# Kernel optimization log

Measured on AMD Instinct MI355X. Metric: run time of the kernel, lower is better.

## Reference

```python
import jax, jax.numpy as jnp
import numpy as np

RF = 13          # receptive field with defaults
N_LAYERS = 8     # blocks(4) * layers(2)
DIMS = 32
RC = 16          # residual/dilation channels
SC = 8           # skip channels
BN_EPS = 1e-5


def conv1x1(x, W, b=None):
    # x: (B,Cin,N,T), W: (Cout,Cin)
    y = jnp.einsum('oc,bcnt->bont', W, x)
    if b is not None:
        y = y + b[None, :, None, None]
    return y


def bn_eval(x, g, b):
    # eval-mode BatchNorm2d with running_mean=0, running_var=1
    return x * (g / jnp.sqrt(1.0 + BN_EPS))[None, :, None, None] + b[None, :, None, None]


def setup_inputs() -> dict:
    key = jax.random.key(0)
    ks = jax.random.split(key, 24)
    B, N, T, days = 16, 1024, 12, 288
    inp = {}
    inp['inputs'] = jax.random.normal(ks[0], (B, 2, N, T), dtype=jnp.float32)
    inp['ind'] = jax.random.randint(ks[1], (B,), 0, days)
    # start convs (1 -> RC)
    inp['start_w'] = jax.random.normal(ks[2], (RC, 1)) * 0.05
    inp['start_b'] = jax.random.normal(ks[3], (RC,)) * 0.05
    inp['starta_w'] = jax.random.normal(ks[4], (RC, 1)) * 0.05
    inp['starta_b'] = jax.random.normal(ks[5], (RC,)) * 0.05
    # dynamic-graph node embeddings (torch.randn init)
    inp['p1'] = jax.random.normal(ks[6], (days, DIMS))
    inp['p2'] = jax.random.normal(ks[7], (N, DIMS))
    inp['p3'] = jax.random.normal(ks[8], (N, DIMS))
    inp['pk'] = jax.random.normal(ks[9], (DIMS, DIMS, DIMS))
    # shared channel-attention fcs (bias=False)
    inp['fc1_w'] = jax.random.normal(ks[10], (RC, RC)) * 0.05
    inp['fc2_w'] = jax.random.normal(ks[11], (RC, RC)) * 0.05
    # per-layer skip convs (RC -> SC)
    inp['skip_w'] = jax.random.normal(ks[12], (N_LAYERS, SC, RC)) * 0.05
    inp['skip_b'] = jax.random.normal(ks[13], (N_LAYERS, SC)) * 0.05
    # per-layer gcn mlp ((order*support_len+1)*RC = 48 -> RC)
    inp['gconv_w'] = jax.random.normal(ks[14], (N_LAYERS, RC, 3 * RC)) * 0.05
    inp['gconv_b'] = jax.random.normal(ks[15], (N_LAYERS, RC)) * 0.05
    # batchnorm affine params
    inp['bn_g'] = jnp.ones((N_LAYERS, RC)) + jax.random.normal(ks[16], (N_LAYERS, RC)) * 0.01
    inp['bn_b'] = jax.random.normal(ks[17], (N_LAYERS, RC)) * 0.01
    inp['bna_g'] = jnp.ones((N_LAYERS, RC)) + jax.random.normal(ks[18], (N_LAYERS, RC)) * 0.01
    inp['bna_b'] = jax.random.normal(ks[19], (N_LAYERS, RC)) * 0.01
    # end convs: 832 -> 64 -> 12
    inp['end1_w'] = jax.random.normal(ks[20], (64, SC * RF * N_LAYERS)) * 0.02
    inp['end1_b'] = jax.random.normal(ks[21], (64,)) * 0.02
    inp['end2_w'] = jax.random.normal(ks[22], (12, 64)) * 0.02
    inp['end2_b'] = jax.random.normal(ks[23], (12,)) * 0.02
    return inp


def reference(inputs, ind, start_w, start_b, starta_w, starta_b, p1, p2, p3, pk,
              fc1_w, fc2_w, skip_w, skip_b, gconv_w, gconv_b,
              bn_g, bn_b, bna_g, bna_b, end1_w, end1_b, end2_w, end2_b):
    B, _, N, T = inputs.shape
    if T < RF:  # static python condition
        xo = jnp.pad(inputs, ((0, 0), (0, 0), (0, 0), (RF - T, 0)))
    else:
        xo = inputs
    x = conv1x1(xo[:, 0:1], start_w, start_b)      # (B,RC,N,RF)
    x_a = conv1x1(xo[:, 1:2], starta_w, starta_b)  # (B,RC,N,RF)

    # dgconstruct: dynamic adjacency (identical for every layer -> compute once)
    te = p1[ind]                                   # (B,DIMS)
    adp = jnp.einsum('ai,ijk->ajk', te, pk)        # (B,DIMS,DIMS)
    src = jnp.einsum('bj,ajk->abk', p2, adp)       # (B,N,DIMS)
    full = jnp.einsum('ck,abk->abc', p3, src)      # (B,N,N)
    temp = full[:, :, :DIMS]                       # (B,N,DIMS)
    x1 = jnp.einsum('bnd,bmd->bnm', src, temp)     # (B,N,N)
    A = jax.nn.relu(jnp.tanh(x1 - jnp.swapaxes(x1, 1, 2)))  # x2 = x1^T

    skips = []
    for i in range(N_LAYERS):
        residual = x
        # avg-pool / max-pool to same size are identity -> avg_out == max_out
        a_out = conv1x1(jax.nn.relu(conv1x1(residual, fc1_w)), fc2_w)
        x = jax.nn.sigmoid(a_out + a_out + x)
        residual_a = x_a
        s = conv1x1(x, skip_w[i], skip_b[i])        # (B,SC,N,RF)
        skips.append(jnp.transpose(s, (0, 1, 3, 2)).reshape(B, SC * RF, N, 1))
        # gcn with support_len=1, order=2 (dropout off in eval)
        h1 = jnp.einsum('bcvl,bwv->bcwl', x, A)
        h2 = jnp.einsum('bcvl,bwv->bcwl', h1, A)
        h = jnp.concatenate([x, h1, h2], axis=1)    # (B,3*RC,N,RF)
        x = conv1x1(h, gconv_w[i], gconv_b[i])
        x = x_a + x
        x_a = x_a + residual_a
        x = x + residual
        x = bn_eval(x, bn_g[i], bn_b[i])
        x_a = bn_eval(x_a, bna_g[i], bna_b[i])

    # torch prepends each new skip: last layer's skip goes first
    skip = jnp.concatenate(skips[::-1], axis=1)     # (B,832,N,1)
    out = jax.nn.relu(skip)
    out = jax.nn.relu(conv1x1(out, end1_w, end1_b))
    out = conv1x1(out, end2_w, end2_b)              # (B,12,N,1)
    return out
```

## Files before the change

### kernel.cpp

```cpp
#include <hip/hip_runtime.h>
#include <math.h>

#define NB 16
#define NCH 16
#define NL 13
#define NN 1024
#define NT 12
#define NLAY 8
#define MROWS 208
#define MPAD 256

typedef _Float16 f16;
typedef __attribute__((ext_vector_type(8))) _Float16 f16x8;
typedef __attribute__((ext_vector_type(16))) float f32x16;

#define OFF_TAB   0
#define OFF_ADP   1024
#define OFF_M     (OFF_ADP  + (size_t)NB*1024)
#define OFF_SRC   (OFF_M    + (size_t)NB*1024)
#define OFF_TEMP  (OFF_SRC  + (size_t)NB*NN*32)
#define OFF_AH    (OFF_TEMP + (size_t)NB*NN*32)
#define OFF_XH    (OFF_AH   + (size_t)NB*NN*NN/2)
#define OFF_XL    (OFF_XH   + (size_t)NB*MPAD*NN/2)
#define OFF_H1H   (OFF_XL   + (size_t)NB*MPAD*NN/2)
#define OFF_H1L   (OFF_H1H  + (size_t)NB*MPAD*NN/2)
#define OFF_H2    (OFF_H1L  + (size_t)NB*MPAD*NN/2)
#define OFF_X     (OFF_H2   + (size_t)NB*MPAD*NN)
#define OFF_SKIP  (OFF_X    + (size_t)NB*MROWS*NN)
#define WS_FLOATS (OFF_SKIP + (size_t)NB*832*NN)

__device__ __forceinline__ void gload16(const void* g, void* l) {
    __builtin_amdgcn_global_load_lds(
        (const __attribute__((address_space(1))) unsigned int*)g,
        (__attribute__((address_space(3))) unsigned int*)l,
        16, 0, 0);
}

__device__ __forceinline__ float fast_tanh(float x) {
    float e = __expf(2.0f * x);
    return 1.0f - 2.0f / (e + 1.0f);
}

__global__ void k_tables(const float* __restrict__ bn_g,
                         const float* __restrict__ bna_g, const float* __restrict__ bna_b,
                         const float* __restrict__ sa_w, const float* __restrict__ sa_b,
                         float* __restrict__ tab) {
    int c = threadIdx.x;
    if (c >= 16) return;
    float inv = 1.0f / sqrtf(1.0f + 1e-5f);
    float A = sa_w[c], Bc = sa_b[c];
    for (int i = 0; i < NLAY; i++) {
        tab[i*16 + c]       = bn_g[i*16 + c] * inv;
        tab[128 + i*16 + c] = A;
        tab[256 + i*16 + c] = Bc;
        float ga = bna_g[i*16 + c] * inv;
        A  = 2.0f * ga * A;
        Bc = 2.0f * ga * Bc + bna_b[i*16 + c];
    }
}

__global__ __launch_bounds__(256) void k_startfc(const float* __restrict__ inp,
                        const float* __restrict__ sw, const float* __restrict__ sb,
                        const float* __restrict__ fc1, const float* __restrict__ fc2,
                        const float* __restrict__ skw, const float* __restrict__ skb,
                        float* __restrict__ x, f16* __restrict__ xh, f16* __restrict__ xl,
                        float* __restrict__ skip) {
    int t = threadIdx.x;
    int idx = blockIdx.x*256 + t;
    int n = idx & 1023;
    int q = idx >> 10;
    int l = q % 13, b = q / 13;
    float u = (l == 0) ? 0.f : inp[((size_t)(b*2 + 0)*NN + n)*NT + (l - 1)];
    float v[16], t1[16], v2[16];
    #pragma unroll
    for (int c = 0; c < 16; c++) {
        v[c] = sw[c]*u + sb[c];
        x[((size_t)b*MROWS + c*13 + l)*NN + n] = v[c];
    }
    #pragma unroll
    for (int c = 0; c < 16; c++) {
        float s = 0.f;
        #pragma unroll
        for (int j = 0; j < 16; j++) s += fc1[c*16 + j] * v[j];
        t1[c] = fmaxf(s, 0.f);
    }
    #pragma unroll
    for (int c = 0; c < 16; c++) {
        float s = 0.f;
        #pragma unroll
        for (int j = 0; j < 16; j++) s += fc2[c*16 + j] * t1[j];
        float z = 2.f*s + v[c];
        v2[c] = 1.f / (1.f + __expf(-z));
        size_t o = ((size_t)b*MPAD + c*13 + l)*NN + n;
        f16 hi = (f16)v2[c];
        xh[o] = hi;
        xl[o] = (f16)(v2[c] - (float)hi);
    }
    #pragma unroll
    for (int sc = 0; sc < 8; sc++) {
        float s = skb[sc];
        #pragma unroll
        for (int c = 0; c < 16; c++) s += skw[sc*16 + c] * v2[c];
        skip[((size_t)b*832 + 7*104 + sc*13 + l)*NN + n] = s;
    }
}

__global__ __launch_bounds__(256) void k_adp(const float* __restrict__ p1, const int* __restrict__ ind,
                      const float* __restrict__ pk, const float* __restrict__ p3,
                      float* __restrict__ adpg, float* __restrict__ Mg) {
    __shared__ float te[32];
    __shared__ float adp[32][32];
    __shared__ float p3s[32][32];
    int b = blockIdx.x, t = threadIdx.x;
    if (t < 32) te[t] = p1[(size_t)ind[b]*32 + t];
    for (int i = t; i < 1024; i += 256) p3s[i >> 5][i & 31] = p3[i];
    __syncthreads();
    for (int i = t; i < 1024; i += 256) {
        float s = 0.f;
        for (int q = 0; q < 32; q++) s += te[q] * pk[q*1024 + i];
        adp[i >> 5][i & 31] = s;
        adpg[(size_t)b*1024 + i] = s;
    }
    __syncthreads();
    for (int i = t; i < 1024; i += 256) {
        int j = i >> 5, c = i & 31;
        float s = 0.f;
        for (int k = 0; k < 32; k++) s += adp[j][k] * p3s[c][k];
        Mg[(size_t)b*1024 + i] = s;
    }
}

__global__ __launch_bounds__(256) void k_st(const float* __restrict__ p2, const float* __restrict__ adpg,
                     const float* __restrict__ Mg,
                     float* __restrict__ src, float* __restrict__ temp) {
    __shared__ float adpS[32][32], MS[32][32], p2S[128][32];
    int b = blockIdx.y, n0 = blockIdx.x * 128, t = threadIdx.x;
    for (int i = t; i < 1024; i += 256) {
        adpS[i >> 5][i & 31] = adpg[(size_t)b*1024 + i];
        MS[i >> 5][i & 31]   = Mg[(size_t)b*1024 + i];
    }
    for (int i = t; i < 128*32; i += 256) p2S[i >> 5][i & 31] = p2[(size_t)(n0 + (i >> 5))*32 + (i & 31)];
    __syncthreads();
    int k = t & 31, g = t >> 5;
    for (int nn = g; nn < 128; nn += 8) {
        float rs = 0.f, rt = 0.f;
        #pragma unroll 8
        for (int j = 0; j < 32; j++) {
            float pv = p2S[nn][j];
            rs += pv * adpS[j][k];
            rt += pv * MS[j][k];
        }
        src [((size_t)b*NN + n0 + nn)*32 + k] = rs;
        temp[((size_t)b*NN + n0 + nn)*32 + k] = rt;
    }
}

__global__ __launch_bounds__(256) void k_A(const float* __restrict__ src, const float* __restrict__ temp,
                    f16* __restrict__ Amat) {
    int b = blockIdx.z;
    int r = blockIdx.x, ti = 0;
    while (r >= 16 - ti) { r -= 16 - ti; ti++; }
    int tj = ti + r;
    int n0 = ti*64, m0 = tj*64;
    __shared__ float snT[32][68], tmT[32][68], smT[32][68], tnT[32][68];
    __shared__ f16 At[64][72];
    int t = threadIdx.x;
    const float* sb_ = src  + (size_t)b*NN*32;
    const float* tb_ = temp + (size_t)b*NN*32;
    for (int i = t; i < 64*32; i += 256) {
        int rr = i >> 5, k = i & 31;
        snT[k][rr] = sb_[(n0 + rr)*32 + k];
        tmT[k][rr] = tb_[(m0 + rr)*32 + k];
        smT[k][rr] = sb_[(m0 + rr)*32 + k];
        tnT[k][rr] = tb_[(n0 + rr)*32 + k];
    }
    __syncthreads();
    int tr = (t >> 4) * 4, tc = (t & 15) * 4;
    float acc1[4][4] = {}, acc2[4][4] = {};
    #pragma unroll 4
    for (int k = 0; k < 32; k++) {
        float4 a  = *(const float4*)&snT[k][tr];
        float4 bb = *(const float4*)&tmT[k][tc];
        float4 c2 = *(const float4*)&smT[k][tc];
        float4 d2 = *(const float4*)&tnT[k][tr];
        float av[4] = {a.x, a.y, a.z, a.w};
        float bv[4] = {bb.x, bb.y, bb.z, bb.w};
        float cv[4] = {c2.x, c2.y, c2.z, c2.w};
        float dv[4] = {d2.x, d2.y, d2.z, d2.w};
        #pragma unroll
        for (int i = 0; i < 4; i++)
            #pragma unroll
            for (int jj = 0; jj < 4; jj++) { acc1[i][jj] += av[i]*bv[jj]; acc2[i][jj] += cv[jj]*dv[i]; }
    }
    #pragma unroll
    for (int i = 0; i < 4; i++)
        #pragma unroll
        for (int jj = 0; jj < 4; jj++) {
            float v = fast_tanh(acc1[i][jj] - acc2[i][jj]);
            Amat[((size_t)b*NN + n0 + tr + i)*NN + m0 + tc + jj] = (f16)(v > 0.f ? v : 0.f);
            At[tc + jj][tr + i] = (f16)(-v > 0.f ? -v : 0.f);
        }
    __syncthreads();
    for (int i = t; i < 512; i += 256) {
        int rr = i >> 3, c8 = (i & 7) * 8;
        f16* dst = &Amat[((size_t)b*NN + m0 + rr)*NN + n0 + c8];
        #pragma unroll
        for (int k = 0; k < 8; k++) dst[k] = At[rr][c8 + k];
    }
}

template<bool HOP1>
__global__ __launch_bounds__(256) void k_gmm(const f16* __restrict__ Xh, const f16* __restrict__ Xl,
                     const f16* __restrict__ Ag, float* __restrict__ Cf,
                     f16* __restrict__ Ch, f16* __restrict__ Cl) {
    __shared__ alignas(16) f16 As[2][128*64];
    __shared__ alignas(16) f16 Xs[2][2*64*64];
    const int bid = blockIdx.x;
    const int xcd = bid & 7;
    const int j   = bid >> 3;
    const int b   = xcd + ((j >> 5) << 3);
    const int tile = j & 31;
    const int my  = tile >> 3;
    const int n0  = (tile & 7) * 128;
    const int t = threadIdx.x;
    const int w = t >> 6, lane = t & 63;
    const char* Ab  = (const char*)(Ag + (size_t)b*NN*NN);
    const char* Xhb = (const char*)(Xh + (size_t)b*MPAD*NN);
    const char* Xlb = (const char*)(Xl + (size_t)b*MPAD*NN);

    const char* asrc[4];
    int adst[4];
    const char* xsrc[4];
    int xdst[4];
    {
        const char* Abase = Ab + (size_t)n0*2048;
        const char* Xb0 = Xhb + (size_t)(my*64)*2048;
        const char* Xb1 = Xlb + (size_t)(my*64)*2048;
        #pragma unroll
        for (int rr = 0; rr < 4; ++rr) {
            int q = rr*4 + w;
            int slot = q*64 + lane;
            int row = slot >> 3, ch = slot & 7;
            asrc[rr] = Abase + (size_t)row*2048 + ((ch ^ (row & 7)) << 4);
            adst[rr] = q*1024;
            int xrow = row & 63;
            xsrc[rr] = ((q >> 3) ? Xb1 : Xb0) + (size_t)xrow*2048 + ((ch ^ (xrow & 7)) << 4);
            xdst[rr] = q*1024;
        }
    }

    const int wm = (w >> 1) * 32, wn = (w & 1) * 64;
    const int kh = lane >> 5;
    const int arow = wm + (lane & 31);
    const int brow0 = wn + (lane & 31);
    const int brow1 = brow0 + 32;
    const int swa = arow & 7, swb0 = brow0 & 7, swb1 = brow1 & 7;

    f32x16 acc0 = {}, acc1 = {};

    auto stage = [&](int buf, int it) {
        size_t koff = (size_t)it * 128;
        #pragma unroll
        for (int rr = 0; rr < 4; ++rr)
            gload16(asrc[rr] + koff, (char*)As[buf] + adst[rr]);
        #pragma unroll
        for (int rr = 0; rr < 4; ++rr)
            gload16(xsrc[rr] + koff, (char*)Xs[buf] + xdst[rr]);
    };
    auto compute = [&](int buf) {
        const char* aP0 = (const char*)Xs[buf] + (size_t)arow*128;
        const char* aP1 = aP0 + 8192;
        const char* bP0 = (const char*)As[buf] + (size_t)brow0*128;
        const char* bP1 = (const char*)As[buf] + (size_t)brow1*128;
        #pragma unroll
        for (int s = 0; s < 4; ++s) {
            int cn = s*2 + kh;
            f16x8 ah = *(const f16x8*)(aP0 + ((cn ^ swa) << 4));
            f16x8 al = *(const f16x8*)(aP1 + ((cn ^ swa) << 4));
            f16x8 b0 = *(const f16x8*)(bP0 + ((cn ^ swb0) << 4));
            f16x8 b1 = *(const f16x8*)(bP1 + ((cn ^ swb1) << 4));
            acc0 = __builtin_amdgcn_mfma_f32_32x32x16_f16(ah, b0, acc0, 0, 0, 0);
            acc1 = __builtin_amdgcn_mfma_f32_32x32x16_f16(ah, b1, acc1, 0, 0, 0);
            acc0 = __builtin_amdgcn_mfma_f32_32x32x16_f16(al, b0, acc0, 0, 0, 0);
            acc1 = __builtin_amdgcn_mfma_f32_32x32x16_f16(al, b1, acc1, 0, 0, 0);
        }
    };

    stage(0, 0);
    int cur = 0;
    for (int it = 0; it < 15; ++it) {
        stage(cur ^ 1, it + 1);
        asm volatile("s_waitcnt vmcnt(8)" ::: "memory");
        __builtin_amdgcn_s_barrier();
        compute(cur);
        __builtin_amdgcn_s_barrier();
        cur ^= 1;
    }
    asm volatile("s_waitcnt vmcnt(0)" ::: "memory");
    __builtin_amdgcn_s_barrier();
    compute(cur);

    const int coll = lane & 31;
    #pragma unroll
    for (int reg = 0; reg < 16; ++reg) {
        int m = my*64 + wm + (reg & 3) + 8*(reg >> 2) + 4*kh;
        if (m < MROWS) {
            size_t o0 = ((size_t)b*MPAD + m)*NN + n0 + wn + coll;
            float v0 = acc0[reg], v1 = acc1[reg];
            if (HOP1) {
                f16 h0 = (f16)v0; Ch[o0]      = h0; Cl[o0]      = (f16)(v0 - (float)h0);
                f16 h1 = (f16)v1; Ch[o0 + 32] = h1; Cl[o0 + 32] = (f16)(v1 - (float)h1);
            } else {
                Cf[o0] = v0; Cf[o0 + 32] = v1;
            }
        }
    }
}

__global__ __launch_bounds__(256) void k_epifc(float* __restrict__ x,
                      f16* __restrict__ xh, f16* __restrict__ xl,
                      const f16* __restrict__ h1h, const f16* __restrict__ h1l,
                      const float* __restrict__ h2,
                      const float* __restrict__ inp, const float* __restrict__ gw,
                      const float* __restrict__ gb, const float* __restrict__ bnb,
                      const float* __restrict__ tab,
                      const float* __restrict__ fc1, const float* __restrict__ fc2,
                      const float* __restrict__ skw, const float* __restrict__ skb,
                      float* __restrict__ skip, int layer) {
    int t = threadIdx.x;
    const int nl = layer + 1;
    const float* Wg  = gw  + layer*768;
    const float* GB  = gb  + layer*16;
    const float* BNB = bnb + layer*16;
    const float* BNS = tab + layer*16;
    const float* AC  = tab + 128 + layer*16;
    const float* BC  = tab + 256 + layer*16;
    const float* W3  = skw + nl*128;
    const float* B3  = skb + nl*8;

    int idx = blockIdx.x*256 + t;
    int n = idx & 1023;
    int q = idx >> 10;
    int l = q % 13, b = q / 13;
    float u1 = (l == 0) ? 0.f : inp[((size_t)(b*2 + 1)*NN + n)*NT + (l - 1)];
    float vx[16], v1[16], v2[16], xnew[16];
    #pragma unroll
    for (int c = 0; c < 16; c++) {
        size_t op = ((size_t)b*MPAD + c*13 + l)*NN + n;
        vx[c] = (float)xh[op] + (float)xl[op];
        v1[c] = (float)h1h[op] + (float)h1l[op];
        v2[c] = h2[op];
    }
    #pragma unroll
    for (int o = 0; o < 16; o++) {
        float s = GB[o];
        #pragma unroll
        for (int c = 0; c < 16; c++) s += Wg[o*48 + c]      * vx[c];
        #pragma unroll
        for (int c = 0; c < 16; c++) s += Wg[o*48 + 16 + c] * v1[c];
        #pragma unroll
        for (int c = 0; c < 16; c++) s += Wg[o*48 + 32 + c] * v2[c];
        float xa = AC[o]*u1 + BC[o];
        float vo = x[((size_t)b*MROWS + o*13 + l)*NN + n];
        xnew[o] = BNS[o]*(s + xa + vo) + BNB[o];
    }
    if (layer < 6) {
        #pragma unroll
        for (int o = 0; o < 16; o++)
            x[((size_t)b*MROWS + o*13 + l)*NN + n] = xnew[o];
    }
    float t1[16], vs[16];
    #pragma unroll
    for (int c = 0; c < 16; c++) {
        float s = 0.f;
        #pragma unroll
        for (int j = 0; j < 16; j++) s += fc1[c*16 + j] * xnew[j];
        t1[c] = fmaxf(s, 0.f);
    }
    #pragma unroll
    for (int c = 0; c < 16; c++) {
        float s = 0.f;
        #pragma unroll
        for (int j = 0; j < 16; j++) s += fc2[c*16 + j] * t1[j];
        float z = 2.f*s + xnew[c];
        vs[c] = 1.f / (1.f + __expf(-z));
        if (layer < 6) {
            size_t o = ((size_t)b*MPAD + c*13 + l)*NN + n;
            f16 hi = (f16)vs[c];
            xh[o] = hi;
            xl[o] = (f16)(vs[c] - (float)hi);
        }
    }
    #pragma unroll
    for (int sc = 0; sc < 8; sc++) {
        float s = B3[sc];
        #pragma unroll
        for (int c = 0; c < 16; c++) s += W3[sc*16 + c] * vs[c];
        skip[((size_t)b*832 + (7 - nl)*104 + sc*13 + l)*NN + n] = s;
    }
}

__global__ __launch_bounds__(256) void k_end1(const float* __restrict__ skip, const float* __restrict__ w1,
                       float* __restrict__ out1) {
    __shared__ alignas(16) float Ws[52][68];
    __shared__ alignas(16) float Ss[52][68];
    int n0 = blockIdx.x * 64, ks = blockIdx.y, b = blockIdx.z;
    int t = threadIdx.x, ty = t >> 4, tx = t & 15;
    float acc[4][4] = {};
    int kbase = ks * 208;
    for (int kk = 0; kk < 4; kk++) {
        int k0 = kbase + kk*52;
        for (int i = t; i < 52*64; i += 256) {
            int r = i >> 6, c = i & 63;
            float sv = skip[((size_t)b*832 + k0 + r)*NN + n0 + c];
            Ss[r][c] = sv > 0.f ? sv : 0.f;
            Ws[r][c] = w1[(size_t)c*832 + k0 + r];
        }
        __syncthreads();
        #pragma unroll 4
        for (int k = 0; k < 52; k++) {
            float4 av = *(const float4*)&Ws[k][ty*4];
            float4 bv = *(const float4*)&Ss[k][tx*4];
            float a[4] = {av.x, av.y, av.z, av.w};
            float bb[4] = {bv.x, bv.y, bv.z, bv.w};
            #pragma unroll
            for (int i = 0; i < 4; i++)
                #pragma unroll
                for (int jj = 0; jj < 4; jj++) acc[i][jj] += a[i]*bb[jj];
        }
        __syncthreads();
    }
    #pragma unroll
    for (int i = 0; i < 4; i++)
        #pragma unroll
        for (int jj = 0; jj < 4; jj++)
            out1[(((size_t)ks*NB + b)*64 + ty*4 + i)*NN + n0 + tx*4 + jj] = acc[i][jj];
}

__global__ __launch_bounds__(256) void k_end2(const float* __restrict__ out1, const float* __restrict__ b1,
                       const float* __restrict__ w2, const float* __restrict__ b2,
                       float* __restrict__ outp) {
    __shared__ float S[64][68];
    int n0 = blockIdx.x * 64, b = blockIdx.y;
    int t = threadIdx.x;
    for (int i = t; i < 4096; i += 256) {
        int o = i >> 6, n = i & 63;
        float s = b1[o];
        #pragma unroll
        for (int ks = 0; ks < 4; ks++)
            s += out1[(((size_t)ks*NB + b)*64 + o)*NN + n0 + n];
        S[o][n] = s > 0.f ? s : 0.f;
    }
    __syncthreads();
    for (int idx = t; idx < 12*64; idx += 256) {
        int jr = idx >> 6, n = idx & 63;
        float s = b2[jr];
        for (int o = 0; o < 64; o++) s += w2[jr*64 + o] * S[o][n];
        outp[((size_t)b*12 + jr)*NN + n0 + n] = s;
    }
}

extern "C" void kernel_launch(void* const* d_in, const int* in_sizes, int n_in,
                              void* d_out, int out_size, void* d_ws, size_t ws_size,
                              hipStream_t stream) {
    (void)in_sizes; (void)n_in; (void)out_size;
    if (ws_size < WS_FLOATS * sizeof(float)) return;

    const float* inputs  = (const float*)d_in[0];
    const int*   ind     = (const int*)  d_in[1];
    const float* start_w = (const float*)d_in[2];
    const float* start_b = (const float*)d_in[3];
    const float* starta_w= (const float*)d_in[4];
    const float* starta_b= (const float*)d_in[5];
    const float* p1      = (const float*)d_in[6];
    const float* p2      = (const float*)d_in[7];
    const float* p3      = (const float*)d_in[8];
    const float* pk      = (const float*)d_in[9];
    const float* fc1_w   = (const float*)d_in[10];
    const float* fc2_w   = (const float*)d_in[11];
    const float* skip_w  = (const float*)d_in[12];
    const float* skip_b  = (const float*)d_in[13];
    const float* gconv_w = (const float*)d_in[14];
    const float* gconv_b = (const float*)d_in[15];
    const float* bn_g    = (const float*)d_in[16];
    const float* bn_b    = (const float*)d_in[17];
    const float* bna_g   = (const float*)d_in[18];
    const float* bna_b   = (const float*)d_in[19];
    const float* end1_w  = (const float*)d_in[20];
    const float* end1_b  = (const float*)d_in[21];
    const float* end2_w  = (const float*)d_in[22];
    const float* end2_b  = (const float*)d_in[23];

    float* ws   = (float*)d_ws;
    float* tab  = ws + OFF_TAB;
    float* adpg = ws + OFF_ADP;
    float* Mg   = ws + OFF_M;
    float* src  = ws + OFF_SRC;
    float* temp = ws + OFF_TEMP;
    f16*   Ah   = (f16*)(ws + OFF_AH);
    f16*   xh   = (f16*)(ws + OFF_XH);
    f16*   xl   = (f16*)(ws + OFF_XL);
    f16*   h1h  = (f16*)(ws + OFF_H1H);
    f16*   h1l  = (f16*)(ws + OFF_H1L);
    float* h2   = ws + OFF_H2;
    float* x    = ws + OFF_X;
    float* skip = ws + OFF_SKIP;

    k_tables<<<1, 64, 0, stream>>>(bn_g, bna_g, bna_b, starta_w, starta_b, tab);
    k_startfc<<<(NB*NL*NN)/256, 256, 0, stream>>>(inputs, start_w, start_b, fc1_w, fc2_w,
                                                  skip_w, skip_b, x, xh, xl, skip);
    k_adp<<<NB, 256, 0, stream>>>(p1, ind, pk, p3, adpg, Mg);
    k_st<<<dim3(8, NB), 256, 0, stream>>>(p2, adpg, Mg, src, temp);
    k_A<<<dim3(136, 1, NB), 256, 0, stream>>>(src, temp, Ah);

    for (int i = 0; i < 7; i++) {
        k_gmm<true ><<<512, 256, 0, stream>>>(xh,  xl,  Ah, nullptr, h1h, h1l);
        k_gmm<false><<<512, 256, 0, stream>>>(h1h, h1l, Ah, h2, nullptr, nullptr);
        k_epifc<<<(NB*NL*NN)/256, 256, 0, stream>>>(x, xh, xl, h1h, h1l, h2, inputs,
                                                    gconv_w, gconv_b, bn_b, tab,
                                                    fc1_w, fc2_w, skip_w, skip_b, skip, i);
    }
    k_end1<<<dim3(16, 4, NB), 256, 0, stream>>>(skip, end1_w, h2);
    k_end2<<<dim3(16, NB), 256, 0, stream>>>(h2, end1_b, end2_w, end2_b, (float*)d_out);
}
```

Before: 619.3 us.

## Split epilogue channels across two threads per point and pre-transpose end1 weights

The epilogue kernel now uses two threads per (b,l,n) point. Each thread owns 8 of the 16 channels, and the threads exchange intermediate vectors through shared memory with barriers. This doubles the grid and lowers per-thread register pressure, at the cost of LDS traffic and extra synchronisation. A small kernel also transposes the end1 weight into a k-major layout, so k_end1 loads weights with coalesced accesses instead of strided ones.

```diff
diff --git a/kernel.cpp b/kernel.cpp
--- a/kernel.cpp
+++ b/kernel.cpp
@@ -27,7 +27,8 @@
 #define OFF_H2    (OFF_H1L  + (size_t)NB*MPAD*NN/2)
 #define OFF_X     (OFF_H2   + (size_t)NB*MPAD*NN)
 #define OFF_SKIP  (OFF_X    + (size_t)NB*MROWS*NN)
-#define WS_FLOATS (OFF_SKIP + (size_t)NB*832*NN)
+#define OFF_W1T   (OFF_SKIP + (size_t)NB*832*NN)
+#define WS_FLOATS (OFF_W1T  + (size_t)832*64)
 
 __device__ __forceinline__ void gload16(const void* g, void* l) {
     __builtin_amdgcn_global_load_lds(
@@ -57,6 +58,16 @@
         A  = 2.0f * ga * A;
         Bc = 2.0f * ga * Bc + bna_b[i*16 + c];
     }
+}
+
+__global__ __launch_bounds__(256) void k_wt(const float* __restrict__ w1, float* __restrict__ w1t) {
+    __shared__ float T[64][65];
+    int kb = blockIdx.x * 64;
+    int t = threadIdx.x;
+    int r = t >> 6, cc = t & 63;
+    for (int o = r; o < 64; o += 4) T[o][cc] = w1[(size_t)o*832 + kb + cc];
+    __syncthreads();
+    for (int k = r; k < 64; k += 4) w1t[(size_t)(kb + k)*64 + cc] = T[cc][k];
 }
 
 __global__ __launch_bounds__(256) void k_startfc(const float* __restrict__ inp,
@@ -327,7 +338,14 @@
                       const float* __restrict__ fc1, const float* __restrict__ fc2,
                       const float* __restrict__ skw, const float* __restrict__ skb,
                       float* __restrict__ skip, int layer) {
+    __shared__ float VX[16][128], V1[16][128], V2[16][128];
     int t = threadIdx.x;
+    int p = t & 127, h = t >> 7;
+    int c0 = h*8;
+    int bid = blockIdx.x;
+    int n = ((bid & 7) << 7) + p;
+    int bl = bid >> 3;
+    int l = bl % 13, b = bl / 13;
     const int nl = layer + 1;
     const float* Wg  = gw  + layer*768;
     const float* GB  = gb  + layer*16;
@@ -338,69 +356,87 @@
     const float* W3  = skw + nl*128;
     const float* B3  = skb + nl*8;
 
-    int idx = blockIdx.x*256 + t;
-    int n = idx & 1023;
-    int q = idx >> 10;
-    int l = q % 13, b = q / 13;
+    float vo[8];
+    #pragma unroll
+    for (int i = 0; i < 8; i++) {
+        int c = c0 + i;
+        size_t op = ((size_t)b*MPAD + c*13 + l)*NN + n;
+        VX[c][p] = (float)xh[op] + (float)xl[op];
+        V1[c][p] = (float)h1h[op] + (float)h1l[op];
+        V2[c][p] = h2[op];
+        vo[i] = x[((size_t)b*MROWS + c*13 + l)*NN + n];
+    }
     float u1 = (l == 0) ? 0.f : inp[((size_t)(b*2 + 1)*NN + n)*NT + (l - 1)];
-    float vx[16], v1[16], v2[16], xnew[16];
-    #pragma unroll
-    for (int c = 0; c < 16; c++) {
-        size_t op = ((size_t)b*MPAD + c*13 + l)*NN + n;
-        vx[c] = (float)xh[op] + (float)xl[op];
-        v1[c] = (float)h1h[op] + (float)h1l[op];
-        v2[c] = h2[op];
-    }
-    #pragma unroll
-    for (int o = 0; o < 16; o++) {
+    __syncthreads();
+
+    float xnew[8];
+    #pragma unroll
+    for (int i = 0; i < 8; i++) {
+        int o = c0 + i;
         float s = GB[o];
         #pragma unroll
-        for (int c = 0; c < 16; c++) s += Wg[o*48 + c]      * vx[c];
-        #pragma unroll
-        for (int c = 0; c < 16; c++) s += Wg[o*48 + 16 + c] * v1[c];
-        #pragma unroll
-        for (int c = 0; c < 16; c++) s += Wg[o*48 + 32 + c] * v2[c];
+        for (int c = 0; c < 16; c++) {
+            s += Wg[o*48 + c]      * VX[c][p];
+            s += Wg[o*48 + 16 + c] * V1[c][p];
+            s += Wg[o*48 + 32 + c] * V2[c][p];
+        }
         float xa = AC[o]*u1 + BC[o];
-        float vo = x[((size_t)b*MROWS + o*13 + l)*NN + n];
-        xnew[o] = BNS[o]*(s + xa + vo) + BNB[o];
+        xnew[i] = BNS[o]*(s + xa + vo[i]) + BNB[o];
     }
     if (layer < 6) {
         #pragma unroll
-        for (int o = 0; o < 16; o++)
-            x[((size_t)b*MROWS + o*13 + l)*NN + n] = xnew[o];
-    }
-    float t1[16], vs[16];
-    #pragma unroll
-    for (int c = 0; c < 16; c++) {
+        for (int i = 0; i < 8; i++)
+            x[((size_t)b*MROWS + (c0 + i)*13 + l)*NN + n] = xnew[i];
+    }
+    __syncthreads();
+    #pragma unroll
+    for (int i = 0; i < 8; i++) VX[c0 + i][p] = xnew[i];
+    __syncthreads();
+
+    float t1[8];
+    #pragma unroll
+    for (int i = 0; i < 8; i++) {
+        int c = c0 + i;
         float s = 0.f;
         #pragma unroll
-        for (int j = 0; j < 16; j++) s += fc1[c*16 + j] * xnew[j];
-        t1[c] = fmaxf(s, 0.f);
-    }
-    #pragma unroll
-    for (int c = 0; c < 16; c++) {
+        for (int j = 0; j < 16; j++) s += fc1[c*16 + j] * VX[j][p];
+        t1[i] = fmaxf(s, 0.f);
+    }
+    #pragma unroll
+    for (int i = 0; i < 8; i++) V1[c0 + i][p] = t1[i];
+    __syncthreads();
+
+    float vs[8];
+    #pragma unroll
+    for (int i = 0; i < 8; i++) {
+        int c = c0 + i;
         float s = 0.f;
         #pragma unroll
-        for (int j = 0; j < 16; j++) s += fc2[c*16 + j] * t1[j];
-        float z = 2.f*s + xnew[c];
-        vs[c] = 1.f / (1.f + __expf(-z));
+        for (int j = 0; j < 16; j++) s += fc2[c*16 + j] * V1[j][p];
+        float z = 2.f*s + xnew[i];
+        vs[i] = 1.f / (1.f + __expf(-z));
         if (layer < 6) {
             size_t o = ((size_t)b*MPAD + c*13 + l)*NN + n;
-            f16 hi = (f16)vs[c];
+            f16 hi = (f16)vs[i];
             xh[o] = hi;
-            xl[o] = (f16)(vs[c] - (float)hi);
-        }
-    }
-    #pragma unroll
-    for (int sc = 0; sc < 8; sc++) {
+            xl[o] = (f16)(vs[i] - (float)hi);
+        }
+    }
+    #pragma unroll
+    for (int i = 0; i < 8; i++) V2[c0 + i][p] = vs[i];
+    __syncthreads();
+
+    #pragma unroll
+    for (int i = 0; i < 4; i++) {
+        int sc = h*4 + i;
         float s = B3[sc];
         #pragma unroll
-        for (int c = 0; c < 16; c++) s += W3[sc*16 + c] * vs[c];
+        for (int c = 0; c < 16; c++) s += W3[sc*16 + c] * V2[c][p];
         skip[((size_t)b*832 + (7 - nl)*104 + sc*13 + l)*NN + n] = s;
     }
 }
 
-__global__ __launch_bounds__(256) void k_end1(const float* __restrict__ skip, const float* __restrict__ w1,
+__global__ __launch_bounds__(256) void k_end1(const float* __restrict__ skip, const float* __restrict__ w1t,
                        float* __restrict__ out1) {
     __shared__ alignas(16) float Ws[52][68];
     __shared__ alignas(16) float Ss[52][68];
@@ -414,7 +450,7 @@
             int r = i >> 6, c = i & 63;
             float sv = skip[((size_t)b*832 + k0 + r)*NN + n0 + c];
             Ss[r][c] = sv > 0.f ? sv : 0.f;
-            Ws[r][c] = w1[(size_t)c*832 + k0 + r];
+            Ws[r][c] = w1t[(size_t)(k0 + r)*64 + c];
         }
         __syncthreads();
         #pragma unroll 4
@@ -505,8 +541,10 @@
     float* h2   = ws + OFF_H2;
     float* x    = ws + OFF_X;
     float* skip = ws + OFF_SKIP;
+    float* w1t  = ws + OFF_W1T;
 
     k_tables<<<1, 64, 0, stream>>>(bn_g, bna_g, bna_b, starta_w, starta_b, tab);
+    k_wt<<<13, 256, 0, stream>>>(end1_w, w1t);
     k_startfc<<<(NB*NL*NN)/256, 256, 0, stream>>>(inputs, start_w, start_b, fc1_w, fc2_w,
                                                   skip_w, skip_b, x, xh, xl, skip);
     k_adp<<<NB, 256, 0, stream>>>(p1, ind, pk, p3, adpg, Mg);
@@ -516,10 +554,10 @@
     for (int i = 0; i < 7; i++) {
         k_gmm<true ><<<512, 256, 0, stream>>>(xh,  xl,  Ah, nullptr, h1h, h1l);
         k_gmm<false><<<512, 256, 0, stream>>>(h1h, h1l, Ah, h2, nullptr, nullptr);
-        k_epifc<<<(NB*NL*NN)/256, 256, 0, stream>>>(x, xh, xl, h1h, h1l, h2, inputs,
+        k_epifc<<<(NB*NL*NN)/128, 256, 0, stream>>>(x, xh, xl, h1h, h1l, h2, inputs,
                                                     gconv_w, gconv_b, bn_b, tab,
                                                     fc1_w, fc2_w, skip_w, skip_b, skip, i);
     }
-    k_end1<<<dim3(16, 4, NB), 256, 0, stream>>>(skip, end1_w, h2);
+    k_end1<<<dim3(16, 4, NB), 256, 0, stream>>>(skip, w1t, h2);
     k_end2<<<dim3(16, NB), 256, 0, stream>>>(h2, end1_b, end2_w, end2_b, (float*)d_out);
 }
```

Measured after the change: 746.3 us. +20.5%, slower.
